# Kernel tuning notes

Hardware: AMD Instinct MI355X
Metric: run time of the kernel (lower is better)

Reference implementation:

```python
import jax, jax.numpy as jnp
import numpy as np

N_Q = 4  # QuantumSampler is hard-wired to 4 qubits (16-dim statevector)


def _build_tables():
    """Static permutation for the CNOT chain and Z-sign table, computed once in numpy."""
    n = N_Q
    dim = 1 << n
    cnots = [(i, (i + 1) % n) for i in range(n)]  # (0,1),(1,2),(2,3),(3,0)
    fmap = np.empty(dim, dtype=np.int64)
    for i in range(dim):
        bits = [(i >> (n - 1 - w)) & 1 for w in range(n)]  # wire w <-> bit (n-1-w)
        for c, t in cnots:
            if bits[c]:
                bits[t] ^= 1
        fmap[i] = sum(b << (n - 1 - w) for w, b in enumerate(bits))
    finv = np.argsort(fmap)  # new_state[j] = old_state[finv[j]]
    signs = np.array([[1.0 - 2.0 * ((j >> (n - 1 - w)) & 1) for w in range(n)]
                      for j in range(dim)], dtype=np.float32)  # <Z_w> signs per basis state
    return jnp.asarray(finv), jnp.asarray(signs)

PERM, SIGNS = _build_tables()


def quantum_gate_probs(q, theta):
    """Simulate: RX(q_w) then RX(theta_w) per wire (angles add), CNOT chain, <Z> per wire, softmax.
    q: [B,4] encoder angles; theta: [4] trainable angles. Returns [B,4] gate probabilities."""
    half = 0.5 * (q + theta)                      # RX(a)RX(b) = RX(a+b)
    c = jnp.cos(half).astype(jnp.complex64)       # amplitude on |0>
    s = (jnp.sin(half).astype(jnp.complex64)) * (-1j)  # amplitude on |1> is -i sin(a/2)
    a = jnp.stack([c, s], axis=-1)                # [B,4,2] single-qubit states
    a0, a1, a2, a3 = a[:, 0], a[:, 1], a[:, 2], a[:, 3]
    # product state |psi> = a0 (x) a1 (x) a2 (x) a3  -> [B,2,2,2,2] -> [B,16]
    st = (a0[:, :, None, None, None] * a1[:, None, :, None, None]
          * a2[:, None, None, :, None] * a3[:, None, None, None, :])
    st = st.reshape(q.shape[0], 16)[:, PERM]      # apply CNOT chain (amplitude permutation)
    probs = st.real ** 2 + st.imag ** 2           # [B,16]
    exps = probs @ SIGNS                          # [B,4] Pauli-Z expectations per wire
    return jax.nn.softmax(exps, axis=-1)


def setup_inputs() -> dict:
    key = jax.random.key(0)
    ks = jax.random.split(key, 8)
    T, B, D, H = 256, 128, 1024, 1024
    inputs = jax.random.normal(ks[0], (T, B, D), dtype=jnp.float32)
    sc_d = 1.0 / np.sqrt(D)
    sc_h = 1.0 / np.sqrt(H)
    return {
        "inputs": inputs,
        "Wi": jax.random.normal(ks[1], (H, D), dtype=jnp.float32) * sc_d,
        "bi": jnp.zeros((H,), dtype=jnp.float32),
        "Wh": jax.random.normal(ks[2], (H, H), dtype=jnp.float32) * sc_h,
        "bh": jnp.zeros((H,), dtype=jnp.float32),
        "Wq": jax.random.normal(ks[3], (4, H), dtype=jnp.float32) * sc_h,
        "bq": jnp.zeros((4,), dtype=jnp.float32),
        "theta": jax.random.uniform(ks[4], (4,), dtype=jnp.float32, minval=-np.pi, maxval=np.pi),
    }


def reference(inputs, Wi, bi, Wh, bh, Wq, bq, theta):
    T, B, _ = inputs.shape
    H = Wi.shape[0]
    hx0 = jnp.zeros((B, H), dtype=inputs.dtype)
    cx0 = jnp.zeros((B, H), dtype=inputs.dtype)

    def step(carry, x):
        hx, cx = carry
        combined = x @ Wi.T + bi + hx @ Wh.T + bh   # [B,H]
        qin = combined @ Wq.T + bq                  # [B,4]
        gates = quantum_gate_probs(qin, theta)      # [B,4]
        f, i_, g, o = gates[:, 0:1], gates[:, 1:2], gates[:, 2:3], gates[:, 3:4]
        cx = f * cx + i_ * jnp.tanh(g)              # broadcast [B,1]*[B,H]
        hx = o * jnp.tanh(cx)
        return (hx, cx), hx

    (hx, cx), ys = jax.lax.scan(step, (hx0, cx0), inputs)
    return ys, hx, cx
```

## Files before the change

kernel.cpp:

```cpp
#include <hip/hip_runtime.h>

#define T_STEPS 256
#define BATCH   128
#define DIM     1024
#define NROWS   (T_STEPS * BATCH)

typedef float vfloat4 __attribute__((ext_vector_type(4)));

#define WS_M     0
#define WS_VP    4096
#define WS_QX    8192

__global__ __launch_bounds__(256) void k_prep(const float* __restrict__ Wi,
                                              const float* __restrict__ Wh,
                                              const float* __restrict__ bi,
                                              const float* __restrict__ bh,
                                              const float* __restrict__ Wq,
                                              float* __restrict__ M,
                                              float* __restrict__ vpart) {
    int blk  = blockIdx.x;
    int tid  = threadIdx.x;
    int wave = tid >> 6;
    int lane = tid & 63;

    if (blk < 16) {
        int d = blk * 64 + lane;
        const float* wq = Wq + wave * DIM;
        float acc = 0.f;
        for (int j = 0; j < DIM; j += 8) {
            #pragma unroll
            for (int u = 0; u < 8; u++)
                acc += wq[j + u] * Wi[(size_t)(j + u) * DIM + d];
        }
        M[wave * DIM + d] = acc;
    } else {
        int bb = blk - 16;
        __shared__ float red[4][8];
        int j0 = bb * 16 + wave * 4;
        float sv0 = 0.f, sv1 = 0.f, sv2 = 0.f, sv3 = 0.f;
        float sc0 = 0.f, sc1 = 0.f, sc2 = 0.f, sc3 = 0.f;
        #pragma unroll
        for (int jj = 0; jj < 4; jj++) {
            int j = j0 + jj;
            const float4* row = (const float4*)(Wh + (size_t)j * DIM);
            float s = 0.f;
            #pragma unroll
            for (int k = 0; k < 4; k++) {
                float4 t4 = row[k * 64 + lane];
                s += t4.x + t4.y + t4.z + t4.w;
            }
            #pragma unroll
            for (int off = 32; off; off >>= 1) s += __shfl_xor(s, off, 64);
            float bbias = bi[j] + bh[j];
            float q0 = Wq[0 * DIM + j], q1 = Wq[1 * DIM + j];
            float q2 = Wq[2 * DIM + j], q3 = Wq[3 * DIM + j];
            sv0 += q0 * s;  sc0 += q0 * bbias;
            sv1 += q1 * s;  sc1 += q1 * bbias;
            sv2 += q2 * s;  sc2 += q2 * bbias;
            sv3 += q3 * s;  sc3 += q3 * bbias;
        }
        if (lane == 0) {
            red[wave][0] = sv0; red[wave][1] = sv1; red[wave][2] = sv2; red[wave][3] = sv3;
            red[wave][4] = sc0; red[wave][5] = sc1; red[wave][6] = sc2; red[wave][7] = sc3;
        }
        __syncthreads();
        if (tid < 8)
            vpart[bb * 8 + tid] = red[0][tid] + red[1][tid] + red[2][tid] + red[3][tid];
    }
}

__global__ __launch_bounds__(256) void k_qx(const float* __restrict__ x,
                                            const float* __restrict__ M,
                                            float4* __restrict__ qx4) {
    int gtid   = blockIdx.x * blockDim.x + threadIdx.x;
    int wave   = gtid >> 6;
    int lane   = threadIdx.x & 63;
    int nwaves = (gridDim.x * blockDim.x) >> 6;

    float4 m[4][4];
    #pragma unroll
    for (int w = 0; w < 4; w++)
        #pragma unroll
        for (int k = 0; k < 4; k++)
            m[w][k] = *(const float4*)(M + w * DIM + k * 256 + lane * 4);

    for (int r = wave; r < NROWS; r += nwaves) {
        const float4* row = (const float4*)(x + (size_t)r * DIM);
        float a0 = 0.f, a1 = 0.f, a2 = 0.f, a3 = 0.f;
        #pragma unroll
        for (int k = 0; k < 4; k++) {
            float4 xv = row[k * 64 + lane];
            a0 += xv.x * m[0][k].x + xv.y * m[0][k].y + xv.z * m[0][k].z + xv.w * m[0][k].w;
            a1 += xv.x * m[1][k].x + xv.y * m[1][k].y + xv.z * m[1][k].z + xv.w * m[1][k].w;
            a2 += xv.x * m[2][k].x + xv.y * m[2][k].y + xv.z * m[2][k].z + xv.w * m[2][k].w;
            a3 += xv.x * m[3][k].x + xv.y * m[3][k].y + xv.z * m[3][k].z + xv.w * m[3][k].w;
        }
        #pragma unroll
        for (int off = 32; off; off >>= 1) {
            a0 += __shfl_xor(a0, off, 64);
            a1 += __shfl_xor(a1, off, 64);
            a2 += __shfl_xor(a2, off, 64);
            a3 += __shfl_xor(a3, off, 64);
        }
        if (lane == 0) qx4[r] = make_float4(a0, a1, a2, a3);
    }
}

__device__ __forceinline__ float fast_tanh(float x) {
    float e = __expf(2.f * x);
    return (e - 1.f) * __builtin_amdgcn_rcpf(e + 1.f);
}

__device__ __forceinline__ void rec_step(float4 qv,
                                         float b0, float b1, float b2, float b3,
                                         float v0, float v1, float v2, float v3,
                                         float& h, float& c) {
    float z0 = __cosf(qv.x + b0 + h * v0);
    float z1 = __cosf(qv.y + b1 + h * v1);
    float z2 = __cosf(qv.z + b2 + h * v2);
    float z3 = __cosf(qv.w + b3 + h * v3);
    float e1 = z0 * z1;
    float e2 = e1 * z2;
    float e3 = e2 * z3;
    float e0 = z1 * z2 * z3;
    float x0 = __expf(e0), x1 = __expf(e1), x2 = __expf(e2), x3 = __expf(e3);
    float inv = __builtin_amdgcn_rcpf(x0 + x1 + x2 + x3);
    float f  = x0 * inv;
    float i_ = x1 * inv;
    float g  = x2 * inv;
    float o  = x3 * inv;
    c = f * c + i_ * fast_tanh(g);
    h = o * fast_tanh(c);
}

__global__ __launch_bounds__(64) void k_recw(const float* __restrict__ bq,
                                             const float* __restrict__ theta,
                                             const float* __restrict__ ws,
                                             float* __restrict__ out) {
    const float4* qx4 = (const float4*)(ws + WS_QX);
    const float4* vp4 = (const float4*)(ws + WS_VP);

    const int b    = blockIdx.x & 127;
    const int q    = blockIdx.x >> 7;
    const int lane = threadIdx.x;

    float4 sa = vp4[lane * 2];
    float4 sc = vp4[lane * 2 + 1];
    #pragma unroll
    for (int off = 32; off; off >>= 1) {
        sa.x += __shfl_xor(sa.x, off, 64);  sa.y += __shfl_xor(sa.y, off, 64);
        sa.z += __shfl_xor(sa.z, off, 64);  sa.w += __shfl_xor(sa.w, off, 64);
        sc.x += __shfl_xor(sc.x, off, 64);  sc.y += __shfl_xor(sc.y, off, 64);
        sc.z += __shfl_xor(sc.z, off, 64);  sc.w += __shfl_xor(sc.w, off, 64);
    }
    const float v0 = sa.x, v1 = sa.y, v2 = sa.z, v3 = sa.w;
    const float b0 = sc.x + bq[0] + theta[0];
    const float b1 = sc.y + bq[1] + theta[1];
    const float b2 = sc.z + bq[2] + theta[2];
    const float b3 = sc.w + bq[3] + theta[3];

    float h = 0.f, c = 0.f;

    #define EMIT_H(tt)                                                           \
        do {                                                                     \
            vfloat4 vv = {h, h, h, h};                                           \
            __builtin_nontemporal_store(vv,                                      \
                (vfloat4*)(out + ((size_t)(tt) * BATCH + b) * DIM + q * 256)     \
                    + lane);                                                     \
        } while (0)

    float4 q0 = qx4[0 * BATCH + b], q1 = qx4[1 * BATCH + b];
    float4 q2 = qx4[2 * BATCH + b], q3 = qx4[3 * BATCH + b];
    float4 q4 = qx4[4 * BATCH + b], q5 = qx4[5 * BATCH + b];
    float4 q6 = qx4[6 * BATCH + b], q7 = qx4[7 * BATCH + b];

    for (int t = 0; t < T_STEPS; t += 8) {
        float4 n0, n1, n2, n3, n4, n5, n6, n7;
        if (t + 8 < T_STEPS) {
            n0 = qx4[(t + 8)  * BATCH + b];  n1 = qx4[(t + 9)  * BATCH + b];
            n2 = qx4[(t + 10) * BATCH + b];  n3 = qx4[(t + 11) * BATCH + b];
            n4 = qx4[(t + 12) * BATCH + b];  n5 = qx4[(t + 13) * BATCH + b];
            n6 = qx4[(t + 14) * BATCH + b];  n7 = qx4[(t + 15) * BATCH + b];
        }
        rec_step(q0, b0, b1, b2, b3, v0, v1, v2, v3, h, c); EMIT_H(t + 0);
        rec_step(q1, b0, b1, b2, b3, v0, v1, v2, v3, h, c); EMIT_H(t + 1);
        rec_step(q2, b0, b1, b2, b3, v0, v1, v2, v3, h, c); EMIT_H(t + 2);
        rec_step(q3, b0, b1, b2, b3, v0, v1, v2, v3, h, c); EMIT_H(t + 3);
        rec_step(q4, b0, b1, b2, b3, v0, v1, v2, v3, h, c); EMIT_H(t + 4);
        rec_step(q5, b0, b1, b2, b3, v0, v1, v2, v3, h, c); EMIT_H(t + 5);
        rec_step(q6, b0, b1, b2, b3, v0, v1, v2, v3, h, c); EMIT_H(t + 6);
        rec_step(q7, b0, b1, b2, b3, v0, v1, v2, v3, h, c); EMIT_H(t + 7);
        q0 = n0; q1 = n1; q2 = n2; q3 = n3; q4 = n4; q5 = n5; q6 = n6; q7 = n7;
    }
    #undef EMIT_H

    vfloat4 hv = {h, h, h, h};
    vfloat4 cv = {c, c, c, c};
    __builtin_nontemporal_store(hv,
        (vfloat4*)(out + ((size_t)NROWS + b) * DIM + q * 256) + lane);
    __builtin_nontemporal_store(cv,
        (vfloat4*)(out + ((size_t)NROWS + BATCH + b) * DIM + q * 256) + lane);
}

extern "C" void kernel_launch(void* const* d_in, const int* in_sizes, int n_in,
                              void* d_out, int out_size, void* d_ws, size_t ws_size,
                              hipStream_t stream) {
    const float* inputs = (const float*)d_in[0];
    const float* Wi     = (const float*)d_in[1];
    const float* bi     = (const float*)d_in[2];
    const float* Wh     = (const float*)d_in[3];
    const float* bh     = (const float*)d_in[4];
    const float* Wq     = (const float*)d_in[5];
    const float* bq     = (const float*)d_in[6];
    const float* theta  = (const float*)d_in[7];
    float* out = (float*)d_out;
    float* ws  = (float*)d_ws;

    float*  M     = ws + WS_M;
    float*  vpart = ws + WS_VP;
    float4* qx4   = (float4*)(ws + WS_QX);

    k_prep<<<80,   256, 0, stream>>>(Wi, Wh, bi, bh, Wq, M, vpart);
    k_qx  <<<1024, 256, 0, stream>>>(inputs, M, qx4);
    k_recw<<<512,  64,  0, stream>>>(bq, theta, ws, out);
}
```

Measured before the change: 318.4 us.

## Fuse input projection into recurrence kernel, one block per batch row

```diff
diff --git a/kernel.cpp b/kernel.cpp
--- a/kernel.cpp
+++ b/kernel.cpp
@@ -9,7 +9,6 @@
 
 #define WS_M     0
 #define WS_VP    4096
-#define WS_QX    8192
 
 __global__ __launch_bounds__(256) void k_prep(const float* __restrict__ Wi,
                                               const float* __restrict__ Wh,
@@ -66,43 +65,6 @@
         __syncthreads();
         if (tid < 8)
             vpart[bb * 8 + tid] = red[0][tid] + red[1][tid] + red[2][tid] + red[3][tid];
-    }
-}
-
-__global__ __launch_bounds__(256) void k_qx(const float* __restrict__ x,
-                                            const float* __restrict__ M,
-                                            float4* __restrict__ qx4) {
-    int gtid   = blockIdx.x * blockDim.x + threadIdx.x;
-    int wave   = gtid >> 6;
-    int lane   = threadIdx.x & 63;
-    int nwaves = (gridDim.x * blockDim.x) >> 6;
-
-    float4 m[4][4];
-    #pragma unroll
-    for (int w = 0; w < 4; w++)
-        #pragma unroll
-        for (int k = 0; k < 4; k++)
-            m[w][k] = *(const float4*)(M + w * DIM + k * 256 + lane * 4);
-
-    for (int r = wave; r < NROWS; r += nwaves) {
-        const float4* row = (const float4*)(x + (size_t)r * DIM);
-        float a0 = 0.f, a1 = 0.f, a2 = 0.f, a3 = 0.f;
-        #pragma unroll
-        for (int k = 0; k < 4; k++) {
-            float4 xv = row[k * 64 + lane];
-            a0 += xv.x * m[0][k].x + xv.y * m[0][k].y + xv.z * m[0][k].z + xv.w * m[0][k].w;
-            a1 += xv.x * m[1][k].x + xv.y * m[1][k].y + xv.z * m[1][k].z + xv.w * m[1][k].w;
-            a2 += xv.x * m[2][k].x + xv.y * m[2][k].y + xv.z * m[2][k].z + xv.w * m[2][k].w;
-            a3 += xv.x * m[3][k].x + xv.y * m[3][k].y + xv.z * m[3][k].z + xv.w * m[3][k].w;
-        }
-        #pragma unroll
-        for (int off = 32; off; off >>= 1) {
-            a0 += __shfl_xor(a0, off, 64);
-            a1 += __shfl_xor(a1, off, 64);
-            a2 += __shfl_xor(a2, off, 64);
-            a3 += __shfl_xor(a3, off, 64);
-        }
-        if (lane == 0) qx4[r] = make_float4(a0, a1, a2, a3);
     }
 }
 
@@ -133,16 +95,52 @@
     h = o * fast_tanh(c);
 }
 
-__global__ __launch_bounds__(64) void k_recw(const float* __restrict__ bq,
-                                             const float* __restrict__ theta,
-                                             const float* __restrict__ ws,
-                                             float* __restrict__ out) {
-    const float4* qx4 = (const float4*)(ws + WS_QX);
+__global__ __launch_bounds__(512) void k_main(const float* __restrict__ x,
+                                              const float* __restrict__ bq,
+                                              const float* __restrict__ theta,
+                                              const float* __restrict__ ws,
+                                              float* __restrict__ out)
+{
+    __shared__ float4 qrow[T_STEPS];
+    const float*  M   = ws + WS_M;
     const float4* vp4 = (const float4*)(ws + WS_VP);
 
-    const int b    = blockIdx.x & 127;
-    const int q    = blockIdx.x >> 7;
-    const int lane = threadIdx.x;
+    const int b    = blockIdx.x;
+    const int tid  = threadIdx.x;
+    const int wave = tid >> 6;
+    const int lane = tid & 63;
+
+    {
+        float4 m[4][4];
+        #pragma unroll
+        for (int w = 0; w < 4; w++)
+            #pragma unroll
+            for (int k = 0; k < 4; k++)
+                m[w][k] = *(const float4*)(M + w * DIM + k * 256 + lane * 4);
+
+        for (int t = wave; t < T_STEPS; t += 8) {
+            const float4* row = (const float4*)(x + ((size_t)t * BATCH + b) * DIM);
+            float a0 = 0.f, a1 = 0.f, a2 = 0.f, a3 = 0.f;
+            #pragma unroll
+            for (int k = 0; k < 4; k++) {
+                float4 xv = row[k * 64 + lane];
+                a0 += xv.x * m[0][k].x + xv.y * m[0][k].y + xv.z * m[0][k].z + xv.w * m[0][k].w;
+                a1 += xv.x * m[1][k].x + xv.y * m[1][k].y + xv.z * m[1][k].z + xv.w * m[1][k].w;
+                a2 += xv.x * m[2][k].x + xv.y * m[2][k].y + xv.z * m[2][k].z + xv.w * m[2][k].w;
+                a3 += xv.x * m[3][k].x + xv.y * m[3][k].y + xv.z * m[3][k].z + xv.w * m[3][k].w;
+            }
+            #pragma unroll
+            for (int off = 32; off; off >>= 1) {
+                a0 += __shfl_xor(a0, off, 64);
+                a1 += __shfl_xor(a1, off, 64);
+                a2 += __shfl_xor(a2, off, 64);
+                a3 += __shfl_xor(a3, off, 64);
+            }
+            if (lane == 0) qrow[t] = make_float4(a0, a1, a2, a3);
+        }
+    }
+    __syncthreads();
+    if (wave >= 4) return;
 
     float4 sa = vp4[lane * 2];
     float4 sc = vp4[lane * 2 + 1];
@@ -165,22 +163,20 @@
         do {                                                                     \
             vfloat4 vv = {h, h, h, h};                                           \
             __builtin_nontemporal_store(vv,                                      \
-                (vfloat4*)(out + ((size_t)(tt) * BATCH + b) * DIM + q * 256)     \
+                (vfloat4*)(out + ((size_t)(tt) * BATCH + b) * DIM + wave * 256)  \
                     + lane);                                                     \
         } while (0)
 
-    float4 q0 = qx4[0 * BATCH + b], q1 = qx4[1 * BATCH + b];
-    float4 q2 = qx4[2 * BATCH + b], q3 = qx4[3 * BATCH + b];
-    float4 q4 = qx4[4 * BATCH + b], q5 = qx4[5 * BATCH + b];
-    float4 q6 = qx4[6 * BATCH + b], q7 = qx4[7 * BATCH + b];
+    float4 q0 = qrow[0], q1 = qrow[1], q2 = qrow[2], q3 = qrow[3];
+    float4 q4 = qrow[4], q5 = qrow[5], q6 = qrow[6], q7 = qrow[7];
 
     for (int t = 0; t < T_STEPS; t += 8) {
         float4 n0, n1, n2, n3, n4, n5, n6, n7;
         if (t + 8 < T_STEPS) {
-            n0 = qx4[(t + 8)  * BATCH + b];  n1 = qx4[(t + 9)  * BATCH + b];
-            n2 = qx4[(t + 10) * BATCH + b];  n3 = qx4[(t + 11) * BATCH + b];
-            n4 = qx4[(t + 12) * BATCH + b];  n5 = qx4[(t + 13) * BATCH + b];
-            n6 = qx4[(t + 14) * BATCH + b];  n7 = qx4[(t + 15) * BATCH + b];
+            n0 = qrow[t + 8];  n1 = qrow[t + 9];
+            n2 = qrow[t + 10]; n3 = qrow[t + 11];
+            n4 = qrow[t + 12]; n5 = qrow[t + 13];
+            n6 = qrow[t + 14]; n7 = qrow[t + 15];
         }
         rec_step(q0, b0, b1, b2, b3, v0, v1, v2, v3, h, c); EMIT_H(t + 0);
         rec_step(q1, b0, b1, b2, b3, v0, v1, v2, v3, h, c); EMIT_H(t + 1);
@@ -197,9 +193,9 @@
     vfloat4 hv = {h, h, h, h};
     vfloat4 cv = {c, c, c, c};
     __builtin_nontemporal_store(hv,
-        (vfloat4*)(out + ((size_t)NROWS + b) * DIM + q * 256) + lane);
+        (vfloat4*)(out + ((size_t)NROWS + b) * DIM + wave * 256) + lane);
     __builtin_nontemporal_store(cv,
-        (vfloat4*)(out + ((size_t)NROWS + BATCH + b) * DIM + q * 256) + lane);
+        (vfloat4*)(out + ((size_t)NROWS + BATCH + b) * DIM + wave * 256) + lane);
 }
 
 extern "C" void kernel_launch(void* const* d_in, const int* in_sizes, int n_in,
@@ -216,11 +212,9 @@
     float* out = (float*)d_out;
     float* ws  = (float*)d_ws;
 
-    float*  M     = ws + WS_M;
-    float*  vpart = ws + WS_VP;
-    float4* qx4   = (float4*)(ws + WS_QX);
-
-    k_prep<<<80,   256, 0, stream>>>(Wi, Wh, bi, bh, Wq, M, vpart);
-    k_qx  <<<1024, 256, 0, stream>>>(inputs, M, qx4);
-    k_recw<<<512,  64,  0, stream>>>(bq, theta, ws, out);
-}
+    float* M     = ws + WS_M;
+    float* vpart = ws + WS_VP;
+
+    k_prep<<<80,    256, 0, stream>>>(Wi, Wh, bi, bh, Wq, M, vpart);
+    k_main<<<BATCH, 512, 0, stream>>>(inputs, bq, theta, ws, out);
+}
```

Result: faster. 305.2 us (-4.2%).
